# Performance work log

Hardware: AMD Instinct MI355X
Metric: run time of the kernel (lower is better)

## Reference

```python
import jax, jax.numpy as jnp
import numpy as np

EMBED_DIM = 768
N_HEADS = 12
HEAD_DIM = EMBED_DIM // N_HEADS


def setup_inputs() -> dict:
    key = jax.random.key(0)
    ks = jax.random.split(key, 5)
    s = 1.0 / np.sqrt(EMBED_DIM)
    x = jax.random.normal(ks[0], (8, 1024, EMBED_DIM), dtype=jnp.float32)
    w_qkv = jax.random.normal(ks[1], (EMBED_DIM, 3 * EMBED_DIM), dtype=jnp.float32) * s
    b_qkv = jnp.zeros((3 * EMBED_DIM,), dtype=jnp.float32)
    w_proj = jax.random.normal(ks[2], (EMBED_DIM, EMBED_DIM), dtype=jnp.float32) * s
    b_proj = jnp.zeros((EMBED_DIM,), dtype=jnp.float32)
    return {"x": x, "w_qkv": w_qkv, "b_qkv": b_qkv, "w_proj": w_proj, "b_proj": b_proj}


def reference(x, w_qkv, b_qkv, w_proj, b_proj):
    B, S, D = x.shape
    H, Hd = N_HEADS, HEAD_DIM
    qkv = x @ w_qkv + b_qkv                      # [B,S,3D]
    qkv = qkv.reshape(B, S, 3, H, Hd).transpose(2, 0, 3, 1, 4)  # [3,B,H,S,Hd]
    q, k, v = qkv[0], qkv[1], qkv[2]
    scale = Hd ** -0.5
    attn = jnp.einsum('bhqd,bhkd->bhqk', q, k) * scale  # [B,H,S,S]
    attn = jax.nn.softmax(attn, axis=-1)
    out = jnp.einsum('bhqk,bhkd->bhqd', attn, v)        # [B,H,S,Hd]
    out = out.transpose(0, 2, 1, 3).reshape(B, S, D)
    return out @ w_proj + b_proj
```

## Files before the change

kernel.cpp:

```cpp
#include <hip/hip_runtime.h>
#include <stdint.h>

typedef unsigned short ushort_t;
typedef __bf16 bf16x8 __attribute__((ext_vector_type(8)));
typedef float floatx4 __attribute__((ext_vector_type(4)));

#define B_   8
#define S_   1024
#define D_   768
#define H_   12
#define M_   (B_ * S_)
#define N3_  (3 * D_)
#define QK_  1536

static __device__ __forceinline__ void gl_lds16(const void* g, void* l) {
  __builtin_amdgcn_global_load_lds((const __attribute__((address_space(1))) void*)g,
                                   (__attribute__((address_space(3))) void*)l,
                                   16, 0, 0);
}

static __device__ __forceinline__ ushort_t f2bf(float f) {
  __bf16 h = (__bf16)f;
  return __builtin_bit_cast(unsigned short, h);
}

static __device__ __forceinline__ void store_out(ushort_t* p, float v) { *p = f2bf(v); }
static __device__ __forceinline__ void store_out(float* p, float v) { *p = v; }

__global__ __launch_bounds__(256) void cvt_f32_bf16(const float* __restrict__ in,
                                                    ushort_t* __restrict__ out, int n) {
  const int i = blockIdx.x * 256 + threadIdx.x;
  if (i < n) out[i] = f2bf(in[i]);
}

__global__ __launch_bounds__(256) void transpose_f32_bf16(const float* __restrict__ W,
                                                          ushort_t* __restrict__ Wt,
                                                          int K, int N) {
  __shared__ float tile[32][33];
  const int n0 = blockIdx.x * 32, k0 = blockIdx.y * 32;
  const int tx = threadIdx.x & 31, ty = threadIdx.x >> 5;
#pragma unroll
  for (int i = 0; i < 4; ++i)
    tile[ty + i * 8][tx] = W[(size_t)(k0 + ty + i * 8) * N + n0 + tx];
  __syncthreads();
#pragma unroll
  for (int i = 0; i < 4; ++i)
    Wt[(size_t)(n0 + ty + i * 8) * K + k0 + tx] = f2bf(tile[tx][ty + i * 8]);
}

template <typename OutT, bool SPLITV>
__global__ __launch_bounds__(256) void gemm_bt_bias(const ushort_t* __restrict__ A,
                                                    const ushort_t* __restrict__ Bt,
                                                    const float* __restrict__ bias,
                                                    OutT* __restrict__ C, int CN,
                                                    ushort_t* __restrict__ vt) {
  __shared__ __align__(16) ushort_t As[128 * 32];
  __shared__ __align__(16) ushort_t Bs[128 * 32];
  const int t = threadIdx.x;
  const int wave = t >> 6, lane = t & 63;
  const int quad = lane >> 4, l15 = lane & 15;
  const int wm = wave >> 1, wn = wave & 1;
  const int m0 = blockIdx.y * 128, n0 = blockIdx.x * 128;

  floatx4 acc[4][4];
#pragma unroll
  for (int i = 0; i < 4; ++i)
#pragma unroll
    for (int j = 0; j < 4; ++j) acc[i][j] = (floatx4)0.0f;

  for (int k0 = 0; k0 < 768; k0 += 32) {
    if (k0) __syncthreads();
#pragma unroll
    for (int c = 0; c < 2; ++c) {
      const int i0 = c * 256 + wave * 64;
      const int i = i0 + lane;
      const int row = i >> 2, cp = i & 3;
      gl_lds16(A + (size_t)(m0 + row) * 768 + k0 + cp * 8, As + i0 * 8);
      gl_lds16(Bt + (size_t)(n0 + row) * 768 + k0 + cp * 8, Bs + i0 * 8);
    }
    __syncthreads();

    bf16x8 af[4], bfr[4];
#pragma unroll
    for (int mi = 0; mi < 4; ++mi)
      af[mi] = *(const bf16x8*)(As + (wm * 64 + mi * 16 + l15) * 32 + quad * 8);
#pragma unroll
    for (int ni = 0; ni < 4; ++ni)
      bfr[ni] = *(const bf16x8*)(Bs + (wn * 64 + ni * 16 + l15) * 32 + quad * 8);
#pragma unroll
    for (int mi = 0; mi < 4; ++mi)
#pragma unroll
      for (int ni = 0; ni < 4; ++ni)
        acc[mi][ni] = __builtin_amdgcn_mfma_f32_16x16x32_bf16(af[mi], bfr[ni], acc[mi][ni], 0, 0, 0);
  }

#pragma unroll
  for (int ni = 0; ni < 4; ++ni) {
    const int colb = n0 + wn * 64 + ni * 16;
    const int col = colb + l15;
    const float bb = bias[col];
    if (SPLITV && colb >= 1536) {
      const int hh = (colb - 1536) >> 6;
      const int d  = ((colb - 1536) & 63) + l15;
      const int bh = (m0 >> 10) * H_ + hh;
      ushort_t* vrow = vt + ((size_t)bh * 64 + d) * 1024 +
                       (m0 & 1023) + wm * 64 + quad * 4;
#pragma unroll
      for (int mi = 0; mi < 4; ++mi) {
        ushort4 pk;
        pk.x = f2bf(acc[mi][ni][0] + bb);
        pk.y = f2bf(acc[mi][ni][1] + bb);
        pk.z = f2bf(acc[mi][ni][2] + bb);
        pk.w = f2bf(acc[mi][ni][3] + bb);
        *(ushort4*)(vrow + mi * 16) = pk;
      }
    } else {
#pragma unroll
      for (int mi = 0; mi < 4; ++mi) {
#pragma unroll
        for (int r = 0; r < 4; ++r) {
          const int row = m0 + wm * 64 + mi * 16 + quad * 4 + r;
          store_out(&C[(size_t)row * CN + col], acc[mi][ni][r] + bb);
        }
      }
    }
  }
}

__global__ __launch_bounds__(256) void attn_kernel(const ushort_t* __restrict__ qk,
                                                   const ushort_t* __restrict__ vt,
                                                   ushort_t* __restrict__ o) {
  __shared__ __align__(16) ushort_t Qs[64 * 64];
  __shared__ __align__(16) ushort_t Ks[64 * 64];
  __shared__ __align__(16) ushort_t Vts[64 * 64];
  __shared__ __align__(16) ushort_t Ps[64 * 72];

  const int t = threadIdx.x;
  const int wave = t >> 6, lane = t & 63;
  const int quad = lane >> 4, l15 = lane & 15;

  const int g = blockIdx.x;
  const int xcd = g & 7, gi = g >> 3;
  const int bh = xcd * 12 + (gi >> 4);
  const int q0 = (gi & 15) * 64;
  const int h = bh % H_;
  const int bS = (bh / H_) * S_;
  const ushort_t* vbase = vt + (size_t)bh * 64 * 1024;

#pragma unroll
  for (int c = 0; c < 2; ++c) {
    const int i0 = c * 256 + wave * 64;
    const int i = i0 + lane;
    const int row = i >> 3, sg = (i & 7) ^ (row & 7);
    gl_lds16(qk + (size_t)(bS + q0 + row) * QK_ + h * 64 + sg * 8, Qs + i0 * 8);
  }
  __syncthreads();

  bf16x8 qf[2];
#pragma unroll
  for (int kb = 0; kb < 2; ++kb)
    qf[kb] = *(const bf16x8*)(Qs + (wave * 16 + l15) * 64 +
                              (((kb * 4 + quad) ^ (l15 & 7)) * 8));

  floatx4 oa[4];
#pragma unroll
  for (int d = 0; d < 4; ++d) oa[d] = (floatx4)0.0f;
  float lsum[4] = {0.0f, 0.0f, 0.0f, 0.0f};

  for (int kv0 = 0; kv0 < S_; kv0 += 64) {
#pragma unroll
    for (int c = 0; c < 2; ++c) {
      const int i0 = c * 256 + wave * 64;
      const int i = i0 + lane;
      const int row = i >> 3, sg = (i & 7) ^ (row & 7);
      gl_lds16(qk + (size_t)(bS + kv0 + row) * QK_ + 768 + h * 64 + sg * 8,
               Ks + i0 * 8);
      gl_lds16(vbase + (size_t)row * 1024 + kv0 + sg * 8, Vts + i0 * 8);
    }
    __syncthreads();

    floatx4 sa[4];
#pragma unroll
    for (int ni = 0; ni < 4; ++ni) sa[ni] = (floatx4)0.0f;
#pragma unroll
    for (int ni = 0; ni < 4; ++ni)
#pragma unroll
      for (int kb = 0; kb < 2; ++kb) {
        bf16x8 kf = *(const bf16x8*)(Ks + (ni * 16 + l15) * 64 +
                                     (((kb * 4 + quad) ^ (l15 & 7)) * 8));
        sa[ni] = __builtin_amdgcn_mfma_f32_16x16x32_bf16(qf[kb], kf, sa[ni], 0, 0, 0);
      }

#pragma unroll
    for (int r = 0; r < 4; ++r) {
      float psum = 0.0f;
#pragma unroll
      for (int ni = 0; ni < 4; ++ni) {
        const float p = __expf(fmaf(sa[ni][r], 0.125f, -16.0f));
        psum += p;
        Ps[(wave * 16 + quad * 4 + r) * 72 + ni * 16 + l15] = f2bf(p);
      }
      lsum[r] += psum;
    }

#pragma unroll
    for (int kb = 0; kb < 2; ++kb) {
      bf16x8 pf = *(const bf16x8*)(Ps + (wave * 16 + l15) * 72 + kb * 32 + quad * 8);
#pragma unroll
      for (int dt = 0; dt < 4; ++dt) {
        bf16x8 vf = *(const bf16x8*)(Vts + (dt * 16 + l15) * 64 +
                                     (((kb * 4 + quad) ^ (l15 & 7)) * 8));
        oa[dt] = __builtin_amdgcn_mfma_f32_16x16x32_bf16(pf, vf, oa[dt], 0, 0, 0);
      }
    }
    __syncthreads();
  }

#pragma unroll
  for (int r = 0; r < 4; ++r) {
#pragma unroll
    for (int off = 8; off >= 1; off >>= 1) lsum[r] += __shfl_xor(lsum[r], off, 64);
  }

#pragma unroll
  for (int dt = 0; dt < 4; ++dt) {
#pragma unroll
    for (int r = 0; r < 4; ++r) {
      const int q = q0 + wave * 16 + quad * 4 + r;
      o[(size_t)(bS + q) * D_ + h * 64 + dt * 16 + l15] = f2bf(oa[dt][r] / lsum[r]);
    }
  }
}

extern "C" void kernel_launch(void* const* d_in, const int* in_sizes, int n_in,
                              void* d_out, int out_size, void* d_ws, size_t ws_size,
                              hipStream_t stream) {
  const float* x      = (const float*)d_in[0];
  const float* w_qkv  = (const float*)d_in[1];
  const float* b_qkv  = (const float*)d_in[2];
  const float* w_proj = (const float*)d_in[3];
  const float* b_proj = (const float*)d_in[4];
  float* out = (float*)d_out;

  ushort_t* xb = (ushort_t*)d_out;

  ushort_t* vtb    = (ushort_t*)d_ws;
  ushort_t* wqkvt  = vtb + (size_t)96 * 64 * 1024;
  ushort_t* wprojt = wqkvt + (size_t)N3_ * D_;
  ushort_t* qkb    = wprojt + (size_t)D_ * D_;
  ushort_t* attnb  = qkb + (size_t)M_ * QK_;

  cvt_f32_bf16<<<(M_ * D_ + 255) / 256, 256, 0, stream>>>(x, xb, M_ * D_);
  transpose_f32_bf16<<<dim3(N3_ / 32, D_ / 32), 256, 0, stream>>>(w_qkv, wqkvt, D_, N3_);
  transpose_f32_bf16<<<dim3(D_ / 32, D_ / 32), 256, 0, stream>>>(w_proj, wprojt, D_, D_);

  gemm_bt_bias<ushort_t, true><<<dim3(N3_ / 128, M_ / 128), 256, 0, stream>>>(
      xb, wqkvt, b_qkv, qkb, QK_, vtb);
  attn_kernel<<<dim3(16 * 96), 256, 0, stream>>>(qkb, vtb, attnb);
  gemm_bt_bias<float, false><<<dim3(D_ / 128, M_ / 128), 256, 0, stream>>>(
      attnb, wprojt, b_proj, out, D_, nullptr);
}
```

Baseline: 216.4 us.

## Double attention query tile to 128 rows and merge prep kernels into one launch

The attention kernel now handles 128 query rows per block, with each wave owning 32 rows across two MFMA row tiles. Each loaded K/V tile is therefore reused across twice as many queries, which halves K/V global traffic and the number of blocks (768 instead of 1536). The three preprocessing kernels (x conversion and the two weight transposes) are folded into a single launch to cut launch overhead. In exchange, the larger tile raises register and LDS use per block, and there are fewer blocks to spread over the CUs.

After: 206.6 us. -4.5%, faster.

```diff
diff --git a/kernel.cpp b/kernel.cpp
--- a/kernel.cpp
+++ b/kernel.cpp
@@ -27,18 +27,13 @@
 static __device__ __forceinline__ void store_out(ushort_t* p, float v) { *p = f2bf(v); }
 static __device__ __forceinline__ void store_out(float* p, float v) { *p = v; }
 
-__global__ __launch_bounds__(256) void cvt_f32_bf16(const float* __restrict__ in,
-                                                    ushort_t* __restrict__ out, int n) {
-  const int i = blockIdx.x * 256 + threadIdx.x;
-  if (i < n) out[i] = f2bf(in[i]);
-}
-
-__global__ __launch_bounds__(256) void transpose_f32_bf16(const float* __restrict__ W,
-                                                          ushort_t* __restrict__ Wt,
-                                                          int K, int N) {
+static __device__ __forceinline__ void transpose_tile(const float* __restrict__ W,
+                                                      ushort_t* __restrict__ Wt,
+                                                      int K, int N, int bx, int by,
+                                                      int t) {
   __shared__ float tile[32][33];
-  const int n0 = blockIdx.x * 32, k0 = blockIdx.y * 32;
-  const int tx = threadIdx.x & 31, ty = threadIdx.x >> 5;
+  const int n0 = bx * 32, k0 = by * 32;
+  const int tx = t & 31, ty = t >> 5;
 #pragma unroll
   for (int i = 0; i < 4; ++i)
     tile[ty + i * 8][tx] = W[(size_t)(k0 + ty + i * 8) * N + n0 + tx];
@@ -46,6 +41,25 @@
 #pragma unroll
   for (int i = 0; i < 4; ++i)
     Wt[(size_t)(n0 + ty + i * 8) * K + k0 + tx] = f2bf(tile[tx][ty + i * 8]);
+}
+
+__global__ __launch_bounds__(256) void prep_kernel(const float* __restrict__ x,
+                                                   ushort_t* __restrict__ xb,
+                                                   const float* __restrict__ w_qkv,
+                                                   ushort_t* __restrict__ wqkvt,
+                                                   const float* __restrict__ w_proj,
+                                                   ushort_t* __restrict__ wprojt) {
+  const int gb = blockIdx.x, t = threadIdx.x;
+  if (gb < 24576) {
+    const int i = gb * 256 + t;
+    xb[i] = f2bf(x[i]);
+  } else if (gb < 24576 + 1728) {
+    const int lb = gb - 24576;
+    transpose_tile(w_qkv, wqkvt, D_, N3_, lb % 72, lb / 72, t);
+  } else {
+    const int lb = gb - 24576 - 1728;
+    transpose_tile(w_proj, wprojt, D_, D_, lb % 24, lb / 24, t);
+  }
 }
 
 template <typename OutT, bool SPLITV>
@@ -130,10 +144,10 @@
 __global__ __launch_bounds__(256) void attn_kernel(const ushort_t* __restrict__ qk,
                                                    const ushort_t* __restrict__ vt,
                                                    ushort_t* __restrict__ o) {
-  __shared__ __align__(16) ushort_t Qs[64 * 64];
+  __shared__ __align__(16) ushort_t Qs[128 * 64];
   __shared__ __align__(16) ushort_t Ks[64 * 64];
   __shared__ __align__(16) ushort_t Vts[64 * 64];
-  __shared__ __align__(16) ushort_t Ps[64 * 72];
+  __shared__ __align__(16) ushort_t Ps[128 * 72];
 
   const int t = threadIdx.x;
   const int wave = t >> 6, lane = t & 63;
@@ -141,14 +155,14 @@
 
   const int g = blockIdx.x;
   const int xcd = g & 7, gi = g >> 3;
-  const int bh = xcd * 12 + (gi >> 4);
-  const int q0 = (gi & 15) * 64;
+  const int bh = xcd * 12 + (gi >> 3);
+  const int q0 = (gi & 7) * 128;
   const int h = bh % H_;
   const int bS = (bh / H_) * S_;
   const ushort_t* vbase = vt + (size_t)bh * 64 * 1024;
 
 #pragma unroll
-  for (int c = 0; c < 2; ++c) {
+  for (int c = 0; c < 4; ++c) {
     const int i0 = c * 256 + wave * 64;
     const int i = i0 + lane;
     const int row = i >> 3, sg = (i & 7) ^ (row & 7);
@@ -156,16 +170,20 @@
   }
   __syncthreads();
 
-  bf16x8 qf[2];
-#pragma unroll
-  for (int kb = 0; kb < 2; ++kb)
-    qf[kb] = *(const bf16x8*)(Qs + (wave * 16 + l15) * 64 +
-                              (((kb * 4 + quad) ^ (l15 & 7)) * 8));
-
-  floatx4 oa[4];
-#pragma unroll
-  for (int d = 0; d < 4; ++d) oa[d] = (floatx4)0.0f;
-  float lsum[4] = {0.0f, 0.0f, 0.0f, 0.0f};
+  bf16x8 qf[2][2];
+#pragma unroll
+  for (int mi = 0; mi < 2; ++mi)
+#pragma unroll
+    for (int kb = 0; kb < 2; ++kb)
+      qf[mi][kb] = *(const bf16x8*)(Qs + (wave * 32 + mi * 16 + l15) * 64 +
+                                    (((kb * 4 + quad) ^ (l15 & 7)) * 8));
+
+  floatx4 oa[2][4];
+#pragma unroll
+  for (int mi = 0; mi < 2; ++mi)
+#pragma unroll
+    for (int d = 0; d < 4; ++d) oa[mi][d] = (floatx4)0.0f;
+  float lsum[2][4] = {{0.f, 0.f, 0.f, 0.f}, {0.f, 0.f, 0.f, 0.f}};
 
   for (int kv0 = 0; kv0 < S_; kv0 += 64) {
 #pragma unroll
@@ -179,57 +197,74 @@
     }
     __syncthreads();
 
-    floatx4 sa[4];
-#pragma unroll
-    for (int ni = 0; ni < 4; ++ni) sa[ni] = (floatx4)0.0f;
+    floatx4 sa[2][4];
+#pragma unroll
+    for (int mi = 0; mi < 2; ++mi)
+#pragma unroll
+      for (int ni = 0; ni < 4; ++ni) sa[mi][ni] = (floatx4)0.0f;
 #pragma unroll
     for (int ni = 0; ni < 4; ++ni)
 #pragma unroll
       for (int kb = 0; kb < 2; ++kb) {
-        bf16x8 kf = *(const bf16x8*)(Ks + (ni * 16 + l15) * 64 +
-                                     (((kb * 4 + quad) ^ (l15 & 7)) * 8));
-        sa[ni] = __builtin_amdgcn_mfma_f32_16x16x32_bf16(qf[kb], kf, sa[ni], 0, 0, 0);
-      }
-
+        const bf16x8 kf = *(const bf16x8*)(Ks + (ni * 16 + l15) * 64 +
+                                           (((kb * 4 + quad) ^ (l15 & 7)) * 8));
+#pragma unroll
+        for (int mi = 0; mi < 2; ++mi)
+          sa[mi][ni] = __builtin_amdgcn_mfma_f32_16x16x32_bf16(qf[mi][kb], kf, sa[mi][ni], 0, 0, 0);
+      }
+
+#pragma unroll
+    for (int mi = 0; mi < 2; ++mi)
+#pragma unroll
+      for (int r = 0; r < 4; ++r) {
+        float psum = 0.0f;
+#pragma unroll
+        for (int ni = 0; ni < 4; ++ni) {
+          const float p = __expf(fmaf(sa[mi][ni][r], 0.125f, -16.0f));
+          psum += p;
+          Ps[(wave * 32 + mi * 16 + quad * 4 + r) * 72 + ni * 16 + l15] = f2bf(p);
+        }
+        lsum[mi][r] += psum;
+      }
+
+#pragma unroll
+    for (int kb = 0; kb < 2; ++kb) {
+      bf16x8 vf[4];
+#pragma unroll
+      for (int dt = 0; dt < 4; ++dt)
+        vf[dt] = *(const bf16x8*)(Vts + (dt * 16 + l15) * 64 +
+                                  (((kb * 4 + quad) ^ (l15 & 7)) * 8));
+#pragma unroll
+      for (int mi = 0; mi < 2; ++mi) {
+        const bf16x8 pf = *(const bf16x8*)(Ps + (wave * 32 + mi * 16 + l15) * 72 +
+                                           kb * 32 + quad * 8);
+#pragma unroll
+        for (int dt = 0; dt < 4; ++dt)
+          oa[mi][dt] = __builtin_amdgcn_mfma_f32_16x16x32_bf16(pf, vf[dt], oa[mi][dt], 0, 0, 0);
+      }
+    }
+    __syncthreads();
+  }
+
+#pragma unroll
+  for (int mi = 0; mi < 2; ++mi)
 #pragma unroll
     for (int r = 0; r < 4; ++r) {
-      float psum = 0.0f;
-#pragma unroll
-      for (int ni = 0; ni < 4; ++ni) {
-        const float p = __expf(fmaf(sa[ni][r], 0.125f, -16.0f));
-        psum += p;
-        Ps[(wave * 16 + quad * 4 + r) * 72 + ni * 16 + l15] = f2bf(p);
-      }
-      lsum[r] += psum;
-    }
-
-#pragma unroll
-    for (int kb = 0; kb < 2; ++kb) {
-      bf16x8 pf = *(const bf16x8*)(Ps + (wave * 16 + l15) * 72 + kb * 32 + quad * 8);
-#pragma unroll
-      for (int dt = 0; dt < 4; ++dt) {
-        bf16x8 vf = *(const bf16x8*)(Vts + (dt * 16 + l15) * 64 +
-                                     (((kb * 4 + quad) ^ (l15 & 7)) * 8));
-        oa[dt] = __builtin_amdgcn_mfma_f32_16x16x32_bf16(pf, vf, oa[dt], 0, 0, 0);
-      }
-    }
-    __syncthreads();
-  }
-
-#pragma unroll
-  for (int r = 0; r < 4; ++r) {
-#pragma unroll
-    for (int off = 8; off >= 1; off >>= 1) lsum[r] += __shfl_xor(lsum[r], off, 64);
-  }
-
-#pragma unroll
-  for (int dt = 0; dt < 4; ++dt) {
-#pragma unroll
-    for (int r = 0; r < 4; ++r) {
-      const int q = q0 + wave * 16 + quad * 4 + r;
-      o[(size_t)(bS + q) * D_ + h * 64 + dt * 16 + l15] = f2bf(oa[dt][r] / lsum[r]);
-    }
-  }
+#pragma unroll
+      for (int off = 8; off >= 1; off >>= 1)
+        lsum[mi][r] += __shfl_xor(lsum[mi][r], off, 64);
+    }
+
+#pragma unroll
+  for (int mi = 0; mi < 2; ++mi)
+#pragma unroll
+    for (int dt = 0; dt < 4; ++dt)
+#pragma unroll
+      for (int r = 0; r < 4; ++r) {
+        const int q = q0 + wave * 32 + mi * 16 + quad * 4 + r;
+        o[(size_t)(bS + q) * D_ + h * 64 + dt * 16 + l15] =
+            f2bf(oa[mi][dt][r] / lsum[mi][r]);
+      }
 }
 
 extern "C" void kernel_launch(void* const* d_in, const int* in_sizes, int n_in,
@@ -250,13 +285,11 @@
   ushort_t* qkb    = wprojt + (size_t)D_ * D_;
   ushort_t* attnb  = qkb + (size_t)M_ * QK_;
 
-  cvt_f32_bf16<<<(M_ * D_ + 255) / 256, 256, 0, stream>>>(x, xb, M_ * D_);
-  transpose_f32_bf16<<<dim3(N3_ / 32, D_ / 32), 256, 0, stream>>>(w_qkv, wqkvt, D_, N3_);
-  transpose_f32_bf16<<<dim3(D_ / 32, D_ / 32), 256, 0, stream>>>(w_proj, wprojt, D_, D_);
-
+  prep_kernel<<<24576 + 1728 + 576, 256, 0, stream>>>(x, xb, w_qkv, wqkvt,
+                                                      w_proj, wprojt);
   gemm_bt_bias<ushort_t, true><<<dim3(N3_ / 128, M_ / 128), 256, 0, stream>>>(
       xb, wqkvt, b_qkv, qkb, QK_, vtb);
-  attn_kernel<<<dim3(16 * 96), 256, 0, stream>>>(qkb, vtb, attnb);
+  attn_kernel<<<dim3(768), 256, 0, stream>>>(qkb, vtb, attnb);
   gemm_bt_bias<float, false><<<dim3(D_ / 128, M_ / 128), 256, 0, stream>>>(
       attnb, wprojt, b_proj, out, D_, nullptr);
 }
```
